# Kernel tuning notes

Hardware: AMD Instinct MI355X
Metric: run time of the kernel (lower is better)

## Reference

```python
import jax, jax.numpy as jnp
import numpy as np

D_MODEL = 1024
N_HEADS = 16
SEQ = 512  # == max_seq_len; rel-pos bias requires n_token == max_seq_len


def setup_inputs() -> dict:
    key = jax.random.key(0)
    ks = jax.random.split(key, 12)
    B = 16
    x = jax.random.normal(ks[0], (B, SEQ, D_MODEL), dtype=jnp.float32)
    c = jax.random.normal(ks[1], (B, SEQ, 8), dtype=jnp.float32)  # unused by forward
    s = 1.0 / np.sqrt(D_MODEL)
    Wq = jax.random.normal(ks[2], (D_MODEL, D_MODEL), dtype=jnp.float32) * s
    bq = jnp.zeros((D_MODEL,), dtype=jnp.float32)
    Wk = jax.random.normal(ks[3], (D_MODEL, D_MODEL), dtype=jnp.float32) * s
    bk = jnp.zeros((D_MODEL,), dtype=jnp.float32)
    Wv = jax.random.normal(ks[4], (D_MODEL, D_MODEL), dtype=jnp.float32) * s
    bv = jnp.zeros((D_MODEL,), dtype=jnp.float32)
    Wo = jax.random.normal(ks[5], (D_MODEL, D_MODEL), dtype=jnp.float32) * s
    bo = jnp.zeros((D_MODEL,), dtype=jnp.float32)
    # trunc_normal_(std=0.02) approximated by normal*0.02 (values stay small)
    rel_table = jax.random.normal(ks[6], (2 * SEQ - 1, N_HEADS), dtype=jnp.float32) * 0.02
    return {"x": x, "c": c, "Wq": Wq, "bq": bq, "Wk": Wk, "bk": bk,
            "Wv": Wv, "bv": bv, "Wo": Wo, "bo": bo, "rel_table": rel_table}


def reference(x, c, Wq, bq, Wk, bk, Wv, bv, Wo, bo, rel_table):
    # x: [B, S, D]; c is unused in the original forward
    B, S, D = x.shape
    H = N_HEADS
    dk = D // H
    scale = 1.0 / np.sqrt(dk)

    q = (x @ Wq + bq).reshape(B, S, H, dk)
    k = (x @ Wk + bk).reshape(B, S, H, dk)
    v = (x @ Wv + bv).reshape(B, S, H, dk)

    # scores: [B, H, S, S]
    scores = jnp.einsum('bihd,bjhd->bhij', q, k) * scale

    # relative position bias: index[i,j] = i + (S-1-j), values in [0, 2S-2]
    rel_index = jnp.arange(S)[:, None] + jnp.arange(S - 1, -1, -1)[None, :]  # [S,S]
    bias = rel_table[rel_index]            # [S, S, H]
    scores = scores + jnp.transpose(bias, (2, 0, 1))[None]  # [1,H,S,S]

    # causal_mask=False: original adds False * -1e9 == 0, so no mask term
    probs = jax.nn.softmax(scores, axis=-1)

    out = jnp.einsum('bhij,bjhd->bihd', probs, v).reshape(B, S, D)
    return out @ Wo + bo
```

## Files before the change

kernel.cpp:

```cpp
#include <hip/hip_runtime.h>
#include <hip/hip_bf16.h>
#include <stdint.h>

#define D_MODEL 1024
#define NH 16
#define SEQ 512
#define DK 64
#define BATCH 16
#define M_TOT (BATCH*SEQ)

typedef unsigned short u16;
typedef unsigned int u32;
typedef __attribute__((ext_vector_type(8))) __bf16 bf16x8;
typedef __attribute__((ext_vector_type(4))) u16 ushort4v;
typedef __attribute__((ext_vector_type(4))) float f32x4;

static __device__ __forceinline__ u16 f2bf(float f) {
    union { float f; u32 i; } c; c.f = f;
    return (u16)((c.i + 0x8000u) >> 16);
}
static __device__ __forceinline__ void async_copy16(const void* g, void* l) {
    __builtin_amdgcn_global_load_lds(
        (const __attribute__((address_space(1))) u32*)g,
        (__attribute__((address_space(3))) u32*)l, 16, 0, 0);
}

__global__ __launch_bounds__(256) void convert_f32_bf16(const float* __restrict__ in,
                                                        u16* __restrict__ out) {
    const int i = (blockIdx.x * 256 + threadIdx.x) * 4;
    float4 v = *(const float4*)&in[i];
    ushort4v o;
    o[0] = f2bf(v.x); o[1] = f2bf(v.y); o[2] = f2bf(v.z); o[3] = f2bf(v.w);
    *(ushort4v*)&out[i] = o;
}

__global__ __launch_bounds__(256) void transpose_w3(const float* __restrict__ W0,
                                                    const float* __restrict__ W1,
                                                    const float* __restrict__ W2,
                                                    u16* __restrict__ Wt) {
    __shared__ u16 tile[64][65];
    const int z = blockIdx.z;
    const float* W = (z == 0) ? W0 : (z == 1) ? W1 : W2;
    const int n0 = blockIdx.x * 64, k0 = blockIdx.y * 64;
    const int t = threadIdx.x;
    #pragma unroll
    for (int p = 0; p < 16; ++p) {
        int idx = p * 256 + t;
        int r = idx >> 6, c = idx & 63;
        tile[r][c] = f2bf(W[(size_t)(k0 + r) * D_MODEL + (n0 + c)]);
    }
    __syncthreads();
    #pragma unroll
    for (int p = 0; p < 16; ++p) {
        int idx = p * 256 + t;
        int r = idx >> 6, c = idx & 63;
        Wt[((size_t)z * D_MODEL + n0 + r) * D_MODEL + (k0 + c)] = tile[c][r];
    }
}

__global__ __launch_bounds__(256) void gemm_bt(const u16* __restrict__ A,
                                               const u16* __restrict__ Bt,
                                               const float* __restrict__ b0,
                                               const float* __restrict__ b1,
                                               const float* __restrict__ b2,
                                               void* __restrict__ o0,
                                               void* __restrict__ o1,
                                               void* __restrict__ o2,
                                               int qkv) {
    __shared__ __attribute__((aligned(16))) u16 smem[16896];
    u16* Asm = smem;
    u16* Bsm = smem + 8192;
    const int t = threadIdx.x;
    const int m0 = blockIdx.y * 128, n0 = blockIdx.x * 128;
    const int lane = t & 63, w = t >> 6;
    const int lm = lane & 15, quad = lane >> 4;
    const int wm = w >> 1, wn = w & 1;

    f32x4 acc[4][4];
    #pragma unroll
    for (int i = 0; i < 4; ++i)
        #pragma unroll
        for (int j = 0; j < 4; ++j) acc[i][j] = (f32x4){0.f, 0.f, 0.f, 0.f};

    for (int kt = 0; kt < D_MODEL / 64; ++kt) {
        const int k0 = kt * 64;
        __syncthreads();
        #pragma unroll
        for (int i = 0; i < 4; ++i) {
            int chunk = i * 256 + t;
            int row = chunk >> 3, c = chunk & 7;
            int cs = c ^ (row & 7);
            const u16* src;
            if (qkv) {
                src = A + (size_t)(m0 + row) * D_MODEL + k0 + cs * 8;
            } else {
                const int m = m0 + row, g = kt * 8 + cs;
                const int b = m >> 9, s = m & 511, h = g >> 3;
                src = A + ((size_t)(b * NH + h) * SEQ + s) * DK + (g & 7) * 8;
            }
            async_copy16(src, &Asm[chunk * 8]);
        }
        #pragma unroll
        for (int i = 0; i < 4; ++i) {
            int chunk = i * 256 + t;
            int row = chunk >> 3, c = chunk & 7;
            int cs = c ^ (row & 7);
            async_copy16(Bt + (size_t)(n0 + row) * D_MODEL + k0 + cs * 8, &Bsm[chunk * 8]);
        }
        __syncthreads();
        #pragma unroll
        for (int ks = 0; ks < 64; ks += 32) {
            const int cbase = ks >> 3;
            bf16x8 af[4], bfv[4];
            #pragma unroll
            for (int im = 0; im < 4; ++im) {
                const int row = wm * 64 + im * 16 + lm;
                const int c = (cbase + quad) ^ (row & 7);
                af[im] = *(const bf16x8*)&Asm[row * 64 + c * 8];
            }
            #pragma unroll
            for (int in = 0; in < 4; ++in) {
                const int row = wn * 64 + in * 16 + lm;
                const int c = (cbase + quad) ^ (row & 7);
                bfv[in] = *(const bf16x8*)&Bsm[row * 64 + c * 8];
            }
            #pragma unroll
            for (int im = 0; im < 4; ++im)
                #pragma unroll
                for (int in = 0; in < 4; ++in)
                    acc[im][in] = __builtin_amdgcn_mfma_f32_16x16x32_bf16(
                        af[im], bfv[in], acc[im][in], 0, 0, 0);
        }
    }

    __syncthreads();
    if (qkv) {
        const int sel = n0 >> 10;
        if (sel == 2) {
            #pragma unroll
            for (int in = 0; in < 4; ++in) {
                const int nn = (n0 & 1023) + wn * 64 + in * 16 + lm;
                const float bv = b2[nn];
                const int h = nn >> 6, d = nn & 63;
                #pragma unroll
                for (int im = 0; im < 4; ++im) {
                    const int mb = m0 + wm * 64 + im * 16 + quad * 4;
                    const int b = mb >> 9, s = mb & 511;
                    ushort4v pk;
                    #pragma unroll
                    for (int r = 0; r < 4; ++r) pk[r] = f2bf(acc[im][in][r] + bv);
                    *(ushort4v*)&((u16*)o2)[((size_t)(b * NH + h) * DK + d) * SEQ + s] = pk;
                }
            }
        } else {
            u16* dst = sel ? (u16*)o1 : (u16*)o0;
            const float* bb = sel ? b1 : b0;
            u16 (*Cs)[132] = (u16(*)[132])smem;
            #pragma unroll
            for (int in = 0; in < 4; ++in) {
                const int nl = wn * 64 + in * 16 + lm;
                const float bv = bb[(n0 & 1023) + nl];
                #pragma unroll
                for (int im = 0; im < 4; ++im)
                    #pragma unroll
                    for (int r = 0; r < 4; ++r)
                        Cs[wm * 64 + im * 16 + quad * 4 + r][nl] =
                            f2bf(acc[im][in][r] + bv);
            }
            __syncthreads();
            const int rr = t >> 1, hh = t & 1;
            const int m = m0 + rr;
            const int b = m >> 9, s = m & 511;
            const int h = ((n0 & 1023) >> 6) + hh;
            u16* dp = &dst[((size_t)(b * NH + h) * SEQ + s) * DK];
            #pragma unroll
            for (int c = 0; c < 8; ++c)
                *(uint4*)&dp[c * 8] = *(const uint4*)&Cs[rr][hh * 64 + c * 8];
        }
    } else {
        float (*Cs)[132] = (float(*)[132])smem;
        #pragma unroll
        for (int ph = 0; ph < 2; ++ph) {
            if (wm == ph) {
                #pragma unroll
                for (int in = 0; in < 4; ++in) {
                    const int nl = wn * 64 + in * 16 + lm;
                    const float bv = b0[n0 + nl];
                    #pragma unroll
                    for (int im = 0; im < 4; ++im)
                        #pragma unroll
                        for (int r = 0; r < 4; ++r)
                            Cs[im * 16 + quad * 4 + r][nl] = acc[im][in][r] + bv;
                }
            }
            __syncthreads();
            const int rr = t >> 2, qq = t & 3;
            float* dp = &((float*)o0)[(size_t)(m0 + ph * 64 + rr) * D_MODEL + n0 + qq * 32];
            #pragma unroll
            for (int c = 0; c < 8; ++c)
                *(uint4*)&dp[c * 4] = *(const uint4*)&Cs[rr][qq * 32 + c * 4];
            __syncthreads();
        }
    }
}

__global__ __launch_bounds__(256) void attn_flash(const u16* __restrict__ qg,
                                                  const u16* __restrict__ kg,
                                                  const u16* __restrict__ vTg,
                                                  const float* __restrict__ rel,
                                                  u16* __restrict__ aout) {
    __shared__ __attribute__((aligned(16))) u16 qt[64 * 64];
    __shared__ __attribute__((aligned(16))) u16 kt[2][64 * 64];
    __shared__ __attribute__((aligned(16))) u16 vt[2][64 * 64];
    __shared__ __attribute__((aligned(16))) u16 Pl[4][16][72];
    __shared__ float biasb[576];

    const int t = threadIdx.x;
    const int lane = t & 63, w = t >> 6;
    const int lm = lane & 15, quad = lane >> 4;
    const int F = blockIdx.x;
    const int xcd = F & 7, qti = (F >> 3) & 7, grp = F >> 6;
    const int p = grp * 8 + xcd;
    const int h = p & 15, b = p >> 4;
    const int q0 = qti * 64;
    const size_t bh = (size_t)(b * NH + h);
    const u16* qb = qg + bh * SEQ * DK;
    const u16* kb = kg + bh * SEQ * DK;
    const u16* vb = vTg + bh * DK * SEQ;

    #pragma unroll
    for (int i = 0; i < 2; ++i) {
        const int chunk = i * 256 + t, row = chunk >> 3, c = chunk & 7;
        const int cs = c ^ (row & 7);
        *(uint4*)&qt[chunk * 8] = *(const uint4*)&qb[(q0 + row) * DK + cs * 8];
    }
    for (int u = t; u < 575; u += 256) biasb[u] = rel[(q0 + u) * NH + h];

    #pragma unroll
    for (int i = 0; i < 2; ++i) {
        const int chunk = i * 256 + t, row = chunk >> 3, c = chunk & 7;
        const int cs = c ^ (row & 7);
        async_copy16(kb + row * DK + cs * 8, &kt[0][chunk * 8]);
        async_copy16(vb + row * SEQ + cs * 8, &vt[0][chunk * 8]);
    }

    float lsum[4] = {0.f, 0.f, 0.f, 0.f};
    f32x4 o[4];
    #pragma unroll
    for (int sd = 0; sd < 4; ++sd) o[sd] = (f32x4){0.f, 0.f, 0.f, 0.f};

    const float scale = 0.125f;

    for (int jt = 0; jt < 8; ++jt) {
        __syncthreads();
        const int cur = jt & 1, nxt = cur ^ 1;
        if (jt < 7) {
            const int j1 = (jt + 1) * 64;
            #pragma unroll
            for (int i = 0; i < 2; ++i) {
                const int chunk = i * 256 + t, row = chunk >> 3, c = chunk & 7;
                const int cs = c ^ (row & 7);
                async_copy16(kb + (j1 + row) * DK + cs * 8, &kt[nxt][chunk * 8]);
                async_copy16(vb + row * SEQ + j1 + cs * 8, &vt[nxt][chunk * 8]);
            }
        }
        const int j0 = jt * 64;

        const int ra = w * 16 + lm;
        bf16x8 aq0 = *(const bf16x8*)&qt[ra * 64 + ((quad) ^ (ra & 7)) * 8];
        bf16x8 aq1 = *(const bf16x8*)&qt[ra * 64 + ((4 + quad) ^ (ra & 7)) * 8];
        #pragma unroll
        for (int js = 0; js < 4; ++js) {
            const int rb = js * 16 + lm;
            bf16x8 bk0 = *(const bf16x8*)&kt[cur][rb * 64 + ((quad) ^ (rb & 7)) * 8];
            bf16x8 bk1 = *(const bf16x8*)&kt[cur][rb * 64 + ((4 + quad) ^ (rb & 7)) * 8];
            f32x4 c = (f32x4){0.f, 0.f, 0.f, 0.f};
            c = __builtin_amdgcn_mfma_f32_16x16x32_bf16(aq0, bk0, c, 0, 0, 0);
            c = __builtin_amdgcn_mfma_f32_16x16x32_bf16(aq1, bk1, c, 0, 0, 0);
            const int jg = j0 + js * 16 + lm;
            #pragma unroll
            for (int r = 0; r < 4; ++r) {
                const int rl = w * 16 + quad * 4 + r;
                float e = __expf(c[r] * scale + biasb[rl + 511 - jg]);
                lsum[r] += e;
                Pl[w][quad * 4 + r][js * 16 + lm] = f2bf(e);
            }
        }

        bf16x8 ap0 = *(const bf16x8*)&Pl[w][lm][quad * 8];
        bf16x8 ap1 = *(const bf16x8*)&Pl[w][lm][32 + quad * 8];
        #pragma unroll
        for (int sd = 0; sd < 4; ++sd) {
            const int rv = sd * 16 + lm;
            bf16x8 bv0 = *(const bf16x8*)&vt[cur][rv * 64 + ((quad) ^ (rv & 7)) * 8];
            bf16x8 bv1 = *(const bf16x8*)&vt[cur][rv * 64 + ((4 + quad) ^ (rv & 7)) * 8];
            o[sd] = __builtin_amdgcn_mfma_f32_16x16x32_bf16(ap0, bv0, o[sd], 0, 0, 0);
            o[sd] = __builtin_amdgcn_mfma_f32_16x16x32_bf16(ap1, bv1, o[sd], 0, 0, 0);
        }
    }

    #pragma unroll
    for (int r = 0; r < 4; ++r) {
        float s = lsum[r];
        s += __shfl_xor(s, 1, 64);
        s += __shfl_xor(s, 2, 64);
        s += __shfl_xor(s, 4, 64);
        s += __shfl_xor(s, 8, 64);
        const float rinv = 1.0f / s;
        #pragma unroll
        for (int sd = 0; sd < 4; ++sd)
            Pl[w][quad * 4 + r][sd * 16 + lm] = f2bf(o[sd][r] * rinv);
    }
    const int rowl = lane >> 2, ch = lane & 3;
    u16* dp = aout + bh * SEQ * DK + (size_t)(q0 + w * 16 + rowl) * DK + ch * 16;
    *(uint4*)&dp[0] = *(const uint4*)&Pl[w][rowl][ch * 16];
    *(uint4*)&dp[8] = *(const uint4*)&Pl[w][rowl][ch * 16 + 8];
}

extern "C" void kernel_launch(void* const* d_in, const int* in_sizes, int n_in,
                              void* d_out, int out_size, void* d_ws, size_t ws_size,
                              hipStream_t stream) {
    const float* x   = (const float*)d_in[0];
    const float* Wq  = (const float*)d_in[2];
    const float* bq  = (const float*)d_in[3];
    const float* Wk  = (const float*)d_in[4];
    const float* bk  = (const float*)d_in[5];
    const float* Wv  = (const float*)d_in[6];
    const float* bv  = (const float*)d_in[7];
    const float* Wo  = (const float*)d_in[8];
    const float* bo  = (const float*)d_in[9];
    const float* rel = (const float*)d_in[10];
    float* out = (float*)d_out;

    u16* ws = (u16*)d_ws;
    const size_t WSZ = (size_t)D_MODEL * D_MODEL;
    const size_t TSZ = (size_t)M_TOT * D_MODEL;
    u16* Wt3 = ws;
    u16* xbf = Wt3 + 3 * WSZ;
    u16* qws = xbf + TSZ;
    u16* kws = qws + TSZ;
    u16* vws = kws + TSZ;
    u16* aws = xbf;

    dim3 tb(256);
    convert_f32_bf16<<<dim3(M_TOT * D_MODEL / 1024), tb, 0, stream>>>(x, xbf);
    transpose_w3<<<dim3(16, 16, 3), tb, 0, stream>>>(Wq, Wk, Wv, Wt3);
    gemm_bt<<<dim3(24, 64), tb, 0, stream>>>(xbf, Wt3, bq, bk, bv, qws, kws, vws, 1);
    attn_flash<<<dim3(2048), tb, 0, stream>>>(qws, kws, vws, rel, aws);
    transpose_w3<<<dim3(16, 16, 1), tb, 0, stream>>>(Wo, Wo, Wo, Wt3);
    gemm_bt<<<dim3(8, 64), tb, 0, stream>>>(aws, Wt3, bo, nullptr, nullptr,
                                            (void*)out, nullptr, nullptr, 0);
}
```

Measured before the change: 258.1 us.

## Triple-buffer GEMM with async prefetch and 256x128 tiles using 512 threads

Rewrites the GEMM main loop as a three-slot software pipeline that prefetches the A and B tiles two iterations ahead with async global-to-LDS copies and partial vmcnt waits. Splitting the prefetch across the two k-halves and raising wave priority around the MFMA blocks aims to overlap memory latency with compute. Block tiles grow to 256x128 with 8 waves, which halves the grid and increases B reuse. The cost is about 144KB of LDS per block, which allows only one block per CU despite the launch bounds of 2. The hand-tuned waitcnt counts also depend on exact load ordering, which makes the code fragile.

```diff
diff --git a/kernel.cpp b/kernel.cpp
--- a/kernel.cpp
+++ b/kernel.cpp
@@ -58,20 +58,18 @@
     }
 }
 
-__global__ __launch_bounds__(256) void gemm_bt(const u16* __restrict__ A,
-                                               const u16* __restrict__ Bt,
-                                               const float* __restrict__ b0,
-                                               const float* __restrict__ b1,
-                                               const float* __restrict__ b2,
-                                               void* __restrict__ o0,
-                                               void* __restrict__ o1,
-                                               void* __restrict__ o2,
-                                               int qkv) {
-    __shared__ __attribute__((aligned(16))) u16 smem[16896];
-    u16* Asm = smem;
-    u16* Bsm = smem + 8192;
+__global__ __launch_bounds__(512, 2) void gemm_bt(const u16* __restrict__ A,
+                                                  const u16* __restrict__ Bt,
+                                                  const float* __restrict__ b0,
+                                                  const float* __restrict__ b1,
+                                                  const float* __restrict__ b2,
+                                                  void* __restrict__ o0,
+                                                  void* __restrict__ o1,
+                                                  void* __restrict__ o2,
+                                                  int qkv) {
+    __shared__ __attribute__((aligned(16))) u16 smem[3 * 24576];
     const int t = threadIdx.x;
-    const int m0 = blockIdx.y * 128, n0 = blockIdx.x * 128;
+    const int m0 = blockIdx.y * 256, n0 = blockIdx.x * 128;
     const int lane = t & 63, w = t >> 6;
     const int lm = lane & 15, quad = lane >> 4;
     const int wm = w >> 1, wn = w & 1;
@@ -82,55 +80,94 @@
         #pragma unroll
         for (int j = 0; j < 4; ++j) acc[i][j] = (f32x4){0.f, 0.f, 0.f, 0.f};
 
-    for (int kt = 0; kt < D_MODEL / 64; ++kt) {
-        const int k0 = kt * 64;
-        __syncthreads();
+    auto stageA = [&](int u, int slot) {
+        u16* dst = &smem[slot * 24576];
         #pragma unroll
         for (int i = 0; i < 4; ++i) {
-            int chunk = i * 256 + t;
-            int row = chunk >> 3, c = chunk & 7;
-            int cs = c ^ (row & 7);
+            const int chunk = i * 512 + t;
+            const int row = chunk >> 3;
+            const int cs = (chunk & 7) ^ (row & 7);
             const u16* src;
             if (qkv) {
-                src = A + (size_t)(m0 + row) * D_MODEL + k0 + cs * 8;
+                src = A + (size_t)(m0 + row) * D_MODEL + u * 64 + cs * 8;
             } else {
-                const int m = m0 + row, g = kt * 8 + cs;
-                const int b = m >> 9, s = m & 511, h = g >> 3;
-                src = A + ((size_t)(b * NH + h) * SEQ + s) * DK + (g & 7) * 8;
-            }
-            async_copy16(src, &Asm[chunk * 8]);
-        }
-        #pragma unroll
-        for (int i = 0; i < 4; ++i) {
-            int chunk = i * 256 + t;
-            int row = chunk >> 3, c = chunk & 7;
-            int cs = c ^ (row & 7);
-            async_copy16(Bt + (size_t)(n0 + row) * D_MODEL + k0 + cs * 8, &Bsm[chunk * 8]);
-        }
-        __syncthreads();
-        #pragma unroll
-        for (int ks = 0; ks < 64; ks += 32) {
-            const int cbase = ks >> 3;
-            bf16x8 af[4], bfv[4];
-            #pragma unroll
-            for (int im = 0; im < 4; ++im) {
-                const int row = wm * 64 + im * 16 + lm;
-                const int c = (cbase + quad) ^ (row & 7);
-                af[im] = *(const bf16x8*)&Asm[row * 64 + c * 8];
-            }
-            #pragma unroll
-            for (int in = 0; in < 4; ++in) {
-                const int row = wn * 64 + in * 16 + lm;
-                const int c = (cbase + quad) ^ (row & 7);
-                bfv[in] = *(const bf16x8*)&Bsm[row * 64 + c * 8];
-            }
-            #pragma unroll
-            for (int im = 0; im < 4; ++im)
-                #pragma unroll
-                for (int in = 0; in < 4; ++in)
-                    acc[im][in] = __builtin_amdgcn_mfma_f32_16x16x32_bf16(
-                        af[im], bfv[in], acc[im][in], 0, 0, 0);
-        }
+                const int m = m0 + row;
+                const int b = m >> 9, s = m & 511;
+                src = A + ((size_t)(b * NH + u) * SEQ + s) * DK + cs * 8;
+            }
+            async_copy16(src, &dst[chunk * 8]);
+        }
+    };
+    auto stageB = [&](int u, int slot) {
+        u16* dst = &smem[slot * 24576 + 16384];
+        #pragma unroll
+        for (int i = 0; i < 2; ++i) {
+            const int chunk = i * 512 + t;
+            const int row = chunk >> 3;
+            const int cs = (chunk & 7) ^ (row & 7);
+            async_copy16(Bt + (size_t)(n0 + row) * D_MODEL + u * 64 + cs * 8,
+                         &dst[chunk * 8]);
+        }
+    };
+
+    stageA(0, 0); stageB(0, 0);
+    stageA(1, 1); stageB(1, 1);
+    asm volatile("s_waitcnt vmcnt(6)" ::: "memory");
+    __builtin_amdgcn_s_barrier();
+
+    int cur = 0;
+    for (int tt = 0; tt < 16; ++tt) {
+        const int nslot = (cur >= 1) ? cur - 1 : 2;
+        const u16* As = &smem[cur * 24576];
+        const u16* Bs = &smem[cur * 24576 + 16384];
+
+        bf16x8 af[4], bfv[4];
+        #pragma unroll
+        for (int ii = 0; ii < 4; ++ii) {
+            const int ra = wm * 64 + ii * 16 + lm;
+            af[ii] = *(const bf16x8*)&As[ra * 64 + (quad ^ (ra & 7)) * 8];
+        }
+        #pragma unroll
+        for (int ii = 0; ii < 4; ++ii) {
+            const int rb = wn * 64 + ii * 16 + lm;
+            bfv[ii] = *(const bf16x8*)&Bs[rb * 64 + (quad ^ (rb & 7)) * 8];
+        }
+        if (tt + 2 < 16) stageA(tt + 2, nslot);
+        __builtin_amdgcn_s_barrier();
+        __builtin_amdgcn_s_setprio(1);
+        #pragma unroll
+        for (int im = 0; im < 4; ++im)
+            #pragma unroll
+            for (int in = 0; in < 4; ++in)
+                acc[im][in] = __builtin_amdgcn_mfma_f32_16x16x32_bf16(
+                    af[im], bfv[in], acc[im][in], 0, 0, 0);
+        __builtin_amdgcn_s_setprio(0);
+        __builtin_amdgcn_s_barrier();
+
+        #pragma unroll
+        for (int ii = 0; ii < 4; ++ii) {
+            const int ra = wm * 64 + ii * 16 + lm;
+            af[ii] = *(const bf16x8*)&As[ra * 64 + ((4 + quad) ^ (ra & 7)) * 8];
+        }
+        #pragma unroll
+        for (int ii = 0; ii < 4; ++ii) {
+            const int rb = wn * 64 + ii * 16 + lm;
+            bfv[ii] = *(const bf16x8*)&Bs[rb * 64 + ((4 + quad) ^ (rb & 7)) * 8];
+        }
+        if (tt + 2 < 16) stageB(tt + 2, nslot);
+        __builtin_amdgcn_s_barrier();
+        __builtin_amdgcn_s_setprio(1);
+        #pragma unroll
+        for (int im = 0; im < 4; ++im)
+            #pragma unroll
+            for (int in = 0; in < 4; ++in)
+                acc[im][in] = __builtin_amdgcn_mfma_f32_16x16x32_bf16(
+                    af[im], bfv[in], acc[im][in], 0, 0, 0);
+        __builtin_amdgcn_s_setprio(0);
+        if (tt < 14)       { asm volatile("s_waitcnt vmcnt(6)" ::: "memory"); }
+        else if (tt == 14) { asm volatile("s_waitcnt vmcnt(0)" ::: "memory"); }
+        __builtin_amdgcn_s_barrier();
+        cur = (cur >= 2) ? 0 : cur + 1;
     }
 
     __syncthreads();
@@ -180,7 +217,7 @@
     } else {
         float (*Cs)[132] = (float(*)[132])smem;
         #pragma unroll
-        for (int ph = 0; ph < 2; ++ph) {
+        for (int ph = 0; ph < 4; ++ph) {
             if (wm == ph) {
                 #pragma unroll
                 for (int in = 0; in < 4; ++in) {
@@ -194,11 +231,11 @@
                 }
             }
             __syncthreads();
-            const int rr = t >> 2, qq = t & 3;
-            float* dp = &((float*)o0)[(size_t)(m0 + ph * 64 + rr) * D_MODEL + n0 + qq * 32];
-            #pragma unroll
-            for (int c = 0; c < 8; ++c)
-                *(uint4*)&dp[c * 4] = *(const uint4*)&Cs[rr][qq * 32 + c * 4];
+            const int rr = t >> 3, qq = t & 7;
+            float* dp = &((float*)o0)[(size_t)(m0 + ph * 64 + rr) * D_MODEL + n0 + qq * 16];
+            #pragma unroll
+            for (int c = 0; c < 4; ++c)
+                *(uint4*)&dp[c * 4] = *(const uint4*)&Cs[rr][qq * 16 + c * 4];
             __syncthreads();
         }
     }
@@ -212,7 +249,7 @@
     __shared__ __attribute__((aligned(16))) u16 qt[64 * 64];
     __shared__ __attribute__((aligned(16))) u16 kt[2][64 * 64];
     __shared__ __attribute__((aligned(16))) u16 vt[2][64 * 64];
-    __shared__ __attribute__((aligned(16))) u16 Pl[4][16][72];
+    __shared__ u16 Pl[4][16][72];
     __shared__ float biasb[576];
 
     const int t = threadIdx.x;
@@ -345,9 +382,9 @@
     dim3 tb(256);
     convert_f32_bf16<<<dim3(M_TOT * D_MODEL / 1024), tb, 0, stream>>>(x, xbf);
     transpose_w3<<<dim3(16, 16, 3), tb, 0, stream>>>(Wq, Wk, Wv, Wt3);
-    gemm_bt<<<dim3(24, 64), tb, 0, stream>>>(xbf, Wt3, bq, bk, bv, qws, kws, vws, 1);
+    gemm_bt<<<dim3(24, 32), dim3(512), 0, stream>>>(xbf, Wt3, bq, bk, bv, qws, kws, vws, 1);
     attn_flash<<<dim3(2048), tb, 0, stream>>>(qws, kws, vws, rel, aws);
     transpose_w3<<<dim3(16, 16, 1), tb, 0, stream>>>(Wo, Wo, Wo, Wt3);
-    gemm_bt<<<dim3(8, 64), tb, 0, stream>>>(aws, Wt3, bo, nullptr, nullptr,
-                                            (void*)out, nullptr, nullptr, 0);
-}
+    gemm_bt<<<dim3(8, 32), dim3(512), 0, stream>>>(aws, Wt3, bo, nullptr, nullptr,
+                                                   (void*)out, nullptr, nullptr, 0);
+}
```

After: 265.1 us. +2.7%, slower.

## Rewrite GEMM as 256x256 tile, 512-thread, double-buffered pipelined kernel

Applied to the files above, without the earlier changes.

The bf16 GEMM moves from a 128x128 tile with 256 threads and a single-buffered load to a 256x256 tile with 512 threads (8 waves). The K loop is software-pipelined: half-tiles of A and B are prefetched asynchronously into two LDS buffers, interleaved with MFMA phases, with explicit vmcnt waits, barriers and s_setprio around the MFMA blocks. The V-transpose epilogue now stages through LDS so global writes are coalesced. The goal is better operand reuse and hiding global load latency, at the cost of 128KB of LDS per block, fewer blocks (384 for QKV, 128 for the output projection), and a possible occupancy or tail-effect penalty.

```diff
diff --git a/kernel.cpp b/kernel.cpp
--- a/kernel.cpp
+++ b/kernel.cpp
@@ -58,147 +58,201 @@
     }
 }
 
-__global__ __launch_bounds__(256) void gemm_bt(const u16* __restrict__ A,
-                                               const u16* __restrict__ Bt,
-                                               const float* __restrict__ b0,
-                                               const float* __restrict__ b1,
-                                               const float* __restrict__ b2,
-                                               void* __restrict__ o0,
-                                               void* __restrict__ o1,
-                                               void* __restrict__ o2,
-                                               int qkv) {
-    __shared__ __attribute__((aligned(16))) u16 smem[16896];
-    u16* Asm = smem;
-    u16* Bsm = smem + 8192;
+__global__ __launch_bounds__(512, 2) void gemm_bt(const u16* __restrict__ A,
+                                                  const u16* __restrict__ Bt,
+                                                  const float* __restrict__ b0,
+                                                  const float* __restrict__ b1,
+                                                  const float* __restrict__ b2,
+                                                  void* __restrict__ o0,
+                                                  void* __restrict__ o1,
+                                                  void* __restrict__ o2,
+                                                  int qkv) {
+    __shared__ __attribute__((aligned(16))) u16 smem[65536];
     const int t = threadIdx.x;
-    const int m0 = blockIdx.y * 128, n0 = blockIdx.x * 128;
+    const int m0 = blockIdx.y * 256, n0 = blockIdx.x * 256;
     const int lane = t & 63, w = t >> 6;
     const int lm = lane & 15, quad = lane >> 4;
-    const int wm = w >> 1, wn = w & 1;
-
-    f32x4 acc[4][4];
-    #pragma unroll
-    for (int i = 0; i < 4; ++i)
+    const int wm2 = w >> 2, wn4 = w & 3;
+
+    f32x4 acc[8][4];
+    #pragma unroll
+    for (int i = 0; i < 8; ++i)
         #pragma unroll
         for (int j = 0; j < 4; ++j) acc[i][j] = (f32x4){0.f, 0.f, 0.f, 0.f};
 
-    for (int kt = 0; kt < D_MODEL / 64; ++kt) {
-        const int k0 = kt * 64;
-        __syncthreads();
-        #pragma unroll
-        for (int i = 0; i < 4; ++i) {
-            int chunk = i * 256 + t;
-            int row = chunk >> 3, c = chunk & 7;
-            int cs = c ^ (row & 7);
+    auto stage_half = [&](int type , int half, int kt, int d) {
+        u16* dst = smem + d * 32768 + type * 16384 + half * 8192;
+        #pragma unroll
+        for (int i = 0; i < 2; ++i) {
+            const int idx = i * 512 + t;
+            const int rl = idx >> 3, c = idx & 7;
+            const int cs = c ^ (rl & 7);
             const u16* src;
-            if (qkv) {
-                src = A + (size_t)(m0 + row) * D_MODEL + k0 + cs * 8;
+            const int row = half * 128 + rl;
+            if (type == 0) {
+                if (qkv) {
+                    src = A + (size_t)(m0 + row) * D_MODEL + kt * 64 + cs * 8;
+                } else {
+                    const int m = m0 + row;
+                    src = A + ((size_t)((m >> 9) * NH + kt) * SEQ + (m & 511)) * DK + cs * 8;
+                }
             } else {
-                const int m = m0 + row, g = kt * 8 + cs;
-                const int b = m >> 9, s = m & 511, h = g >> 3;
-                src = A + ((size_t)(b * NH + h) * SEQ + s) * DK + (g & 7) * 8;
-            }
-            async_copy16(src, &Asm[chunk * 8]);
-        }
-        #pragma unroll
-        for (int i = 0; i < 4; ++i) {
-            int chunk = i * 256 + t;
-            int row = chunk >> 3, c = chunk & 7;
-            int cs = c ^ (row & 7);
-            async_copy16(Bt + (size_t)(n0 + row) * D_MODEL + k0 + cs * 8, &Bsm[chunk * 8]);
-        }
-        __syncthreads();
-        #pragma unroll
-        for (int ks = 0; ks < 64; ks += 32) {
-            const int cbase = ks >> 3;
-            bf16x8 af[4], bfv[4];
-            #pragma unroll
-            for (int im = 0; im < 4; ++im) {
-                const int row = wm * 64 + im * 16 + lm;
-                const int c = (cbase + quad) ^ (row & 7);
-                af[im] = *(const bf16x8*)&Asm[row * 64 + c * 8];
-            }
-            #pragma unroll
-            for (int in = 0; in < 4; ++in) {
-                const int row = wn * 64 + in * 16 + lm;
-                const int c = (cbase + quad) ^ (row & 7);
-                bfv[in] = *(const bf16x8*)&Bsm[row * 64 + c * 8];
-            }
-            #pragma unroll
-            for (int im = 0; im < 4; ++im)
-                #pragma unroll
-                for (int in = 0; in < 4; ++in)
-                    acc[im][in] = __builtin_amdgcn_mfma_f32_16x16x32_bf16(
-                        af[im], bfv[in], acc[im][in], 0, 0, 0);
+                src = Bt + (size_t)(n0 + row) * D_MODEL + kt * 64 + cs * 8;
+            }
+            async_copy16(src, &dst[idx * 8]);
+        }
+    };
+
+    stage_half(0, 0, 0, 0); stage_half(0, 1, 0, 0);
+    stage_half(1, 0, 0, 0); stage_half(1, 1, 0, 0);
+    stage_half(0, 0, 1, 1); stage_half(1, 0, 1, 1);
+    asm volatile("s_waitcnt vmcnt(4)" ::: "memory");
+    __builtin_amdgcn_s_barrier();
+
+    bf16x8 a[4][2];
+    bf16x8 bbuf[2][2][2];
+
+    for (int it = 0; it < 8; ++it) {
+        const int k1g = 2 * it + 1, k2g = 2 * it + 2, k3g = 2 * it + 3;
+        #pragma unroll
+        for (int p = 0; p < 8; ++p) {
+            const int tk = p >> 2, d = tk;
+            const int qq = p & 3, mh = qq >> 1, nh = qq & 1;
+            const u16* As = smem + d * 32768 + mh * 8192;
+            const u16* Bs = smem + d * 32768 + 16384 + nh * 8192;
+            if (nh == 0) {
+                #pragma unroll
+                for (int mf = 0; mf < 4; ++mf) {
+                    const int rl = wm2 * 64 + mf * 16 + lm;
+                    #pragma unroll
+                    for (int ks = 0; ks < 2; ++ks)
+                        a[mf][ks] = *(const bf16x8*)&As[rl * 64 + (((ks * 4 + quad)) ^ (rl & 7)) * 8];
+                }
+            }
+            if (mh == 0) {
+                #pragma unroll
+                for (int nf = 0; nf < 2; ++nf) {
+                    const int rl = wn4 * 32 + nf * 16 + lm;
+                    #pragma unroll
+                    for (int ks = 0; ks < 2; ++ks)
+                        bbuf[nh][nf][ks] = *(const bf16x8*)&Bs[rl * 64 + (((ks * 4 + quad)) ^ (rl & 7)) * 8];
+                }
+            }
+            if (p == 0)      stage_half(0, 1, k1g, 1);
+            else if (p == 1) stage_half(1, 1, k1g, 1);
+            else if (p == 2) { if (it < 7) stage_half(0, 0, k2g, 0); }
+            else if (p == 3) { if (it < 7) stage_half(1, 0, k2g, 0); }
+            else if (p == 4) { if (it < 7) stage_half(0, 1, k2g, 0); }
+            else if (p == 5) { if (it < 7) stage_half(1, 1, k2g, 0); }
+            else if (p == 6) { if (it < 7) stage_half(0, 0, k3g, 1); }
+            else             { if (it < 7) stage_half(1, 0, k3g, 1); }
+            __builtin_amdgcn_s_barrier();
+            __builtin_amdgcn_s_setprio(1);
+            #pragma unroll
+            for (int ks = 0; ks < 2; ++ks)
+                #pragma unroll
+                for (int mf = 0; mf < 4; ++mf)
+                    #pragma unroll
+                    for (int nf = 0; nf < 2; ++nf)
+                        acc[mh * 4 + mf][nh * 2 + nf] = __builtin_amdgcn_mfma_f32_16x16x32_bf16(
+                            a[mf][ks], bbuf[nh][nf][ks], acc[mh * 4 + mf][nh * 2 + nf], 0, 0, 0);
+            __builtin_amdgcn_s_setprio(0);
+            if (p == 3) {
+                if (it < 7) { asm volatile("s_waitcnt vmcnt(4)" ::: "memory"); }
+                else        { asm volatile("s_waitcnt vmcnt(0)" ::: "memory"); }
+            }
+            if (p == 7 && it < 7) { asm volatile("s_waitcnt vmcnt(4)" ::: "memory"); }
+            __builtin_amdgcn_s_barrier();
         }
     }
 
     __syncthreads();
     if (qkv) {
         const int sel = n0 >> 10;
+        const int h0 = (n0 & 1023) >> 6;
         if (sel == 2) {
-            #pragma unroll
-            for (int in = 0; in < 4; ++in) {
-                const int nn = (n0 & 1023) + wn * 64 + in * 16 + lm;
-                const float bv = b2[nn];
-                const int h = nn >> 6, d = nn & 63;
-                #pragma unroll
-                for (int im = 0; im < 4; ++im) {
-                    const int mb = m0 + wm * 64 + im * 16 + quad * 4;
-                    const int b = mb >> 9, s = mb & 511;
-                    ushort4v pk;
-                    #pragma unroll
-                    for (int r = 0; r < 4; ++r) pk[r] = f2bf(acc[im][in][r] + bv);
-                    *(ushort4v*)&((u16*)o2)[((size_t)(b * NH + h) * DK + d) * SEQ + s] = pk;
-                }
+            u16 (*Cs)[264] = (u16(*)[264])smem;
+            const int bb_ = m0 >> 9, s0v = m0 & 511;
+            #pragma unroll
+            for (int ch = 0; ch < 2; ++ch) {
+                #pragma unroll
+                for (int nf = 0; nf < 2; ++nf) {
+                    const int j = ch * 2 + nf;
+                    const int nl = wn4 * 32 + nf * 16 + lm;
+                    const float bvv = b2[(n0 & 1023) + ch * 128 + nl];
+                    #pragma unroll
+                    for (int i = 0; i < 8; ++i) {
+                        const int ml = (i >> 2) * 128 + wm2 * 64 + (i & 3) * 16 + quad * 4;
+                        ushort4v pk;
+                        #pragma unroll
+                        for (int r = 0; r < 4; ++r) pk[r] = f2bf(acc[i][j][r] + bvv);
+                        *(ushort4v*)&Cs[nl][ml] = pk;
+                    }
+                }
+                __syncthreads();
+                const int rowl = t >> 2, chk = t & 3;
+                const int h = h0 + ch * 2 + (rowl >> 6), dd = rowl & 63;
+                u16* dp = (u16*)o2 + ((size_t)(bb_ * NH + h) * DK + dd) * SEQ + s0v + chk * 64;
+                #pragma unroll
+                for (int c = 0; c < 8; ++c)
+                    *(uint4*)&dp[c * 8] = *(const uint4*)&Cs[rowl][chk * 64 + c * 8];
+                __syncthreads();
             }
         } else {
             u16* dst = sel ? (u16*)o1 : (u16*)o0;
-            const float* bb = sel ? b1 : b0;
-            u16 (*Cs)[132] = (u16(*)[132])smem;
-            #pragma unroll
-            for (int in = 0; in < 4; ++in) {
-                const int nl = wn * 64 + in * 16 + lm;
-                const float bv = bb[(n0 & 1023) + nl];
-                #pragma unroll
-                for (int im = 0; im < 4; ++im)
-                    #pragma unroll
-                    for (int r = 0; r < 4; ++r)
-                        Cs[wm * 64 + im * 16 + quad * 4 + r][nl] =
-                            f2bf(acc[im][in][r] + bv);
-            }
-            __syncthreads();
-            const int rr = t >> 1, hh = t & 1;
-            const int m = m0 + rr;
-            const int b = m >> 9, s = m & 511;
-            const int h = ((n0 & 1023) >> 6) + hh;
-            u16* dp = &dst[((size_t)(b * NH + h) * SEQ + s) * DK];
-            #pragma unroll
-            for (int c = 0; c < 8; ++c)
-                *(uint4*)&dp[c * 8] = *(const uint4*)&Cs[rr][hh * 64 + c * 8];
-        }
-    } else {
-        float (*Cs)[132] = (float(*)[132])smem;
-        #pragma unroll
-        for (int ph = 0; ph < 2; ++ph) {
-            if (wm == ph) {
-                #pragma unroll
-                for (int in = 0; in < 4; ++in) {
-                    const int nl = wn * 64 + in * 16 + lm;
-                    const float bv = b0[n0 + nl];
-                    #pragma unroll
-                    for (int im = 0; im < 4; ++im)
+            const float* bb2 = sel ? b1 : b0;
+            u16 (*Cs)[264] = (u16(*)[264])smem;
+            #pragma unroll
+            for (int rh = 0; rh < 2; ++rh) {
+                #pragma unroll
+                for (int j = 0; j < 4; ++j) {
+                    const int nl = (j >> 1) * 128 + wn4 * 32 + (j & 1) * 16 + lm;
+                    const float bvv = bb2[(n0 & 1023) + nl];
+                    #pragma unroll
+                    for (int mf = 0; mf < 4; ++mf) {
+                        const int rr = wm2 * 64 + mf * 16 + quad * 4;
                         #pragma unroll
                         for (int r = 0; r < 4; ++r)
-                            Cs[im * 16 + quad * 4 + r][nl] = acc[im][in][r] + bv;
+                            Cs[rr + r][nl] = f2bf(acc[rh * 4 + mf][j][r] + bvv);
+                    }
+                }
+                __syncthreads();
+                const int rr2 = t >> 2, hd = t & 3;
+                const int m = m0 + rh * 128 + rr2;
+                const int b = m >> 9, s = m & 511;
+                const int h = h0 + hd;
+                u16* dp = &dst[((size_t)(b * NH + h) * SEQ + s) * DK];
+                #pragma unroll
+                for (int c = 0; c < 8; ++c)
+                    *(uint4*)&dp[c * 8] = *(const uint4*)&Cs[rr2][hd * 64 + c * 8];
+                __syncthreads();
+            }
+        }
+    } else {
+        float (*Cs)[260] = (float(*)[260])smem;
+        #pragma unroll
+        for (int ph = 0; ph < 4; ++ph) {
+            const int pmh = ph >> 1, pw = ph & 1;
+            if (wm2 == pw) {
+                #pragma unroll
+                for (int j = 0; j < 4; ++j) {
+                    const int nl = (j >> 1) * 128 + wn4 * 32 + (j & 1) * 16 + lm;
+                    const float bvv = b0[n0 + nl];
+                    #pragma unroll
+                    for (int mf = 0; mf < 4; ++mf) {
+                        const int rr = mf * 16 + quad * 4;
+                        #pragma unroll
+                        for (int r = 0; r < 4; ++r)
+                            Cs[rr + r][nl] = acc[pmh * 4 + mf][j][r] + bvv;
+                    }
                 }
             }
             __syncthreads();
-            const int rr = t >> 2, qq = t & 3;
-            float* dp = &((float*)o0)[(size_t)(m0 + ph * 64 + rr) * D_MODEL + n0 + qq * 32];
+            const int rr2 = t >> 3, cc = t & 7;
+            float* dp = &((float*)o0)[(size_t)(m0 + ph * 64 + rr2) * D_MODEL + n0 + cc * 32];
             #pragma unroll
             for (int c = 0; c < 8; ++c)
-                *(uint4*)&dp[c * 4] = *(const uint4*)&Cs[rr][qq * 32 + c * 4];
+                *(uint4*)&dp[c * 4] = *(const uint4*)&Cs[rr2][cc * 32 + c * 4];
             __syncthreads();
         }
     }
@@ -212,7 +266,7 @@
     __shared__ __attribute__((aligned(16))) u16 qt[64 * 64];
     __shared__ __attribute__((aligned(16))) u16 kt[2][64 * 64];
     __shared__ __attribute__((aligned(16))) u16 vt[2][64 * 64];
-    __shared__ __attribute__((aligned(16))) u16 Pl[4][16][72];
+    __shared__ u16 Pl[4][16][72];
     __shared__ float biasb[576];
 
     const int t = threadIdx.x;
@@ -345,9 +399,9 @@
     dim3 tb(256);
     convert_f32_bf16<<<dim3(M_TOT * D_MODEL / 1024), tb, 0, stream>>>(x, xbf);
     transpose_w3<<<dim3(16, 16, 3), tb, 0, stream>>>(Wq, Wk, Wv, Wt3);
-    gemm_bt<<<dim3(24, 64), tb, 0, stream>>>(xbf, Wt3, bq, bk, bv, qws, kws, vws, 1);
+    gemm_bt<<<dim3(12, 32), dim3(512), 0, stream>>>(xbf, Wt3, bq, bk, bv, qws, kws, vws, 1);
     attn_flash<<<dim3(2048), tb, 0, stream>>>(qws, kws, vws, rel, aws);
     transpose_w3<<<dim3(16, 16, 1), tb, 0, stream>>>(Wo, Wo, Wo, Wt3);
-    gemm_bt<<<dim3(8, 64), tb, 0, stream>>>(aws, Wt3, bo, nullptr, nullptr,
-                                            (void*)out, nullptr, nullptr, 0);
-}
+    gemm_bt<<<dim3(4, 32), dim3(512), 0, stream>>>(aws, Wt3, bo, nullptr, nullptr,
+                                                   (void*)out, nullptr, nullptr, 0);
+}
```

Result: slower. 386.7 us (+49.8%).

## Transpose attention MFMA operands and write output in token-major layout

Applied to the files above, without the earlier changes.

Swaps the A/B operands of the QK^T and PV MFMAs so each lane holds four consecutive key columns of one query row. The exp values can then be packed into 8-byte LDS stores, and the row-sum needs a single scalar accumulator with a two-step cross-quad shuffle instead of four accumulators with four shuffles each. The attention output is now written directly in [B,S,D] layout, so the output-projection GEMM loads A with the same simple row-major addressing as the QKV path instead of a per-chunk head-gather. This relies on the attention kernel having b and h in scope and on the launch code matching the new layout; the writes become 32-byte pieces strided by D_MODEL rather than contiguous per head.

```diff
diff --git a/kernel.cpp b/kernel.cpp
--- a/kernel.cpp
+++ b/kernel.cpp
@@ -90,15 +90,7 @@
             int chunk = i * 256 + t;
             int row = chunk >> 3, c = chunk & 7;
             int cs = c ^ (row & 7);
-            const u16* src;
-            if (qkv) {
-                src = A + (size_t)(m0 + row) * D_MODEL + k0 + cs * 8;
-            } else {
-                const int m = m0 + row, g = kt * 8 + cs;
-                const int b = m >> 9, s = m & 511, h = g >> 3;
-                src = A + ((size_t)(b * NH + h) * SEQ + s) * DK + (g & 7) * 8;
-            }
-            async_copy16(src, &Asm[chunk * 8]);
+            async_copy16(A + (size_t)(m0 + row) * D_MODEL + k0 + cs * 8, &Asm[chunk * 8]);
         }
         #pragma unroll
         for (int i = 0; i < 4; ++i) {
@@ -244,7 +236,7 @@
         async_copy16(vb + row * SEQ + cs * 8, &vt[0][chunk * 8]);
     }
 
-    float lsum[4] = {0.f, 0.f, 0.f, 0.f};
+    float lsum = 0.f;
     f32x4 o[4];
     #pragma unroll
     for (int sd = 0; sd < 4; ++sd) o[sd] = (f32x4){0.f, 0.f, 0.f, 0.f};
@@ -275,16 +267,17 @@
             bf16x8 bk0 = *(const bf16x8*)&kt[cur][rb * 64 + ((quad) ^ (rb & 7)) * 8];
             bf16x8 bk1 = *(const bf16x8*)&kt[cur][rb * 64 + ((4 + quad) ^ (rb & 7)) * 8];
             f32x4 c = (f32x4){0.f, 0.f, 0.f, 0.f};
-            c = __builtin_amdgcn_mfma_f32_16x16x32_bf16(aq0, bk0, c, 0, 0, 0);
-            c = __builtin_amdgcn_mfma_f32_16x16x32_bf16(aq1, bk1, c, 0, 0, 0);
-            const int jg = j0 + js * 16 + lm;
+            c = __builtin_amdgcn_mfma_f32_16x16x32_bf16(bk0, aq0, c, 0, 0, 0);
+            c = __builtin_amdgcn_mfma_f32_16x16x32_bf16(bk1, aq1, c, 0, 0, 0);
+            const int bb0 = w * 16 + lm + 511 - j0 - js * 16 - quad * 4;
+            ushort4v pk;
             #pragma unroll
             for (int r = 0; r < 4; ++r) {
-                const int rl = w * 16 + quad * 4 + r;
-                float e = __expf(c[r] * scale + biasb[rl + 511 - jg]);
-                lsum[r] += e;
-                Pl[w][quad * 4 + r][js * 16 + lm] = f2bf(e);
-            }
+                float e = __expf(c[r] * scale + biasb[bb0 - r]);
+                lsum += e;
+                pk[r] = f2bf(e);
+            }
+            *(ushort4v*)&Pl[w][lm][js * 16 + quad * 4] = pk;
         }
 
         bf16x8 ap0 = *(const bf16x8*)&Pl[w][lm][quad * 8];
@@ -294,25 +287,24 @@
             const int rv = sd * 16 + lm;
             bf16x8 bv0 = *(const bf16x8*)&vt[cur][rv * 64 + ((quad) ^ (rv & 7)) * 8];
             bf16x8 bv1 = *(const bf16x8*)&vt[cur][rv * 64 + ((4 + quad) ^ (rv & 7)) * 8];
-            o[sd] = __builtin_amdgcn_mfma_f32_16x16x32_bf16(ap0, bv0, o[sd], 0, 0, 0);
-            o[sd] = __builtin_amdgcn_mfma_f32_16x16x32_bf16(ap1, bv1, o[sd], 0, 0, 0);
-        }
-    }
-
-    #pragma unroll
-    for (int r = 0; r < 4; ++r) {
-        float s = lsum[r];
-        s += __shfl_xor(s, 1, 64);
-        s += __shfl_xor(s, 2, 64);
-        s += __shfl_xor(s, 4, 64);
-        s += __shfl_xor(s, 8, 64);
-        const float rinv = 1.0f / s;
-        #pragma unroll
-        for (int sd = 0; sd < 4; ++sd)
-            Pl[w][quad * 4 + r][sd * 16 + lm] = f2bf(o[sd][r] * rinv);
+            o[sd] = __builtin_amdgcn_mfma_f32_16x16x32_bf16(bv0, ap0, o[sd], 0, 0, 0);
+            o[sd] = __builtin_amdgcn_mfma_f32_16x16x32_bf16(bv1, ap1, o[sd], 0, 0, 0);
+        }
+    }
+
+    float s = lsum;
+    s += __shfl_xor(s, 16, 64);
+    s += __shfl_xor(s, 32, 64);
+    const float rinv = 1.0f / s;
+    #pragma unroll
+    for (int sd = 0; sd < 4; ++sd) {
+        ushort4v pk;
+        #pragma unroll
+        for (int r = 0; r < 4; ++r) pk[r] = f2bf(o[sd][r] * rinv);
+        *(ushort4v*)&Pl[w][lm][sd * 16 + quad * 4] = pk;
     }
     const int rowl = lane >> 2, ch = lane & 3;
-    u16* dp = aout + bh * SEQ * DK + (size_t)(q0 + w * 16 + rowl) * DK + ch * 16;
+    u16* dp = aout + (size_t)(b * SEQ + q0 + w * 16 + rowl) * D_MODEL + h * DK + ch * 16;
     *(uint4*)&dp[0] = *(const uint4*)&Pl[w][rowl][ch * 16];
     *(uint4*)&dp[8] = *(const uint4*)&Pl[w][rowl][ch * 16 + 8];
 }
```

Result: no change. 258.0 us (-0.0%).
